# Kernel tuning notes

Measured on AMD Instinct MI355X. Metric: run time of the kernel, lower is better.

## Reference

```python
import jax, jax.numpy as jnp
import numpy as np

B, T, C = 128, 256, 384   # batch, seq (== BLOCK_SIZE), embed dim
H, D = 6, 64              # heads, head_dim
M = 128                   # memory prefix length
WIN = 64                  # local window


def setup_inputs() -> dict:
    key = jax.random.key(0)
    ks = jax.random.split(key, 6)
    s = 0.02
    return {
        "x": jax.random.normal(ks[0], (B, T, C), jnp.float32),
        "memory": jax.random.normal(ks[1], (M, C), jnp.float32),
        "W_qkv": (jax.random.normal(ks[2], (C, 3 * C), jnp.float32) * s),
        "b_qkv": jnp.zeros((3 * C,), jnp.float32),
        "W_proj": (jax.random.normal(ks[3], (C, C), jnp.float32) * s),
        "b_proj": jnp.zeros((C,), jnp.float32),
        "gate": jnp.ones((C,), jnp.float32),
    }


def reference(x, memory, W_qkv, b_qkv, W_proj, b_proj, gate):
    Bx, Tx, Cx = x.shape
    Mx = memory.shape[0]
    Tt = Tx + Mx

    qkv = x @ W_qkv + b_qkv                      # [B,T,3C]
    q, k, v = jnp.split(qkv, 3, axis=-1)
    mem = jnp.broadcast_to(memory[None], (Bx, Mx, Cx))
    k = jnp.concatenate([mem, k], axis=1)        # [B,Tt,C]
    v = jnp.concatenate([mem, v], axis=1)

    qh = q.reshape(Bx, Tx, H, D)
    kh = k.reshape(Bx, Tt, H, D)
    vh = v.reshape(Bx, Tt, H, D)

    att = jnp.einsum('bqhd,bkhd->bhqk', qh, kh) * (1.0 / jnp.sqrt(jnp.float32(D)))

    # self part (last T columns): causal AND local window; memory prefix unmasked
    i = jnp.arange(Tx)[:, None]
    j = jnp.arange(Tx)[None, :]
    self_mask = (j <= i) & (jnp.abs(i - j) <= WIN)            # [T,T]
    full_mask = jnp.concatenate(
        [jnp.ones((Tx, Mx), bool), self_mask], axis=1)        # [T,Tt]
    att = jnp.where(full_mask[None, None], att, -jnp.inf)
    att = jax.nn.softmax(att, axis=-1)

    y = jnp.einsum('bhqk,bkhd->bqhd', att, vh).reshape(Bx, Tx, Cx)
    return (y * gate) @ W_proj + b_proj
```

## Files before the change

### kernel.cpp

```cpp
#include <hip/hip_runtime.h>

#define B_   128
#define T_   256
#define C_   384
#define H_   6
#define D_   64
#define M_   128
#define WIN_ 64
#define C3_  1152
#define QKS_ 768

typedef unsigned int   uint;
typedef unsigned short ushort;
typedef __attribute__((ext_vector_type(8))) short bf16x8;
typedef __attribute__((ext_vector_type(4))) float f32x4;

#define AS1 __attribute__((address_space(1)))
#define AS3 __attribute__((address_space(3)))
#define MFMA16(a,b,c) __builtin_amdgcn_mfma_f32_16x16x32_bf16((a),(b),(c),0,0,0)

__device__ __forceinline__ ushort f2bf(float f) {
  union { float f; uint u; } c; c.f = f;
  uint x = c.u;
  return (ushort)((x + 0x7fffu + ((x >> 16) & 1u)) >> 16);
}
__device__ __forceinline__ void gload_lds16(const ushort* g, ushort* l) {
  __builtin_amdgcn_global_load_lds((const AS1 uint*)g, (AS3 uint*)l, 16, 0, 0);
}

#define NX4_  ((B_ * T_ * C_) / 4)
#define NM4_  ((M_ * C_) / 4)
#define NMT_  (H_ * 64 * 128)
#define NWQ_  (C_ * C3_)
#define NWP_  (C_ * C_)

__global__ __launch_bounds__(256)
void k_prep(const float* __restrict__ x, const float* __restrict__ memory,
            const float* __restrict__ Wq, const float* __restrict__ Wp,
            ushort* __restrict__ x_bf, ushort* __restrict__ mem_bf,
            ushort* __restrict__ memT, ushort* __restrict__ Wq_t,
            ushort* __restrict__ Wp_t)
{
  int id = blockIdx.x * 256 + threadIdx.x;
  if (id < NX4_) {
    float4 f = ((const float4*)x)[id];
    ushort4 u; u.x = f2bf(f.x); u.y = f2bf(f.y); u.z = f2bf(f.z); u.w = f2bf(f.w);
    *(ushort4*)&x_bf[id * 4] = u;
    return;
  }
  id -= NX4_;
  if (id < NM4_) {
    float4 f = ((const float4*)memory)[id];
    ushort4 u; u.x = f2bf(f.x); u.y = f2bf(f.y); u.z = f2bf(f.z); u.w = f2bf(f.w);
    *(ushort4*)&mem_bf[id * 4] = u;
    return;
  }
  id -= NM4_;
  if (id < NMT_) {
    int k = id & 127;
    int hd = id >> 7;
    int h = hd >> 6, d = hd & 63;
    memT[id] = f2bf(memory[(size_t)k * C_ + h * 64 + d]);
    return;
  }
  id -= NMT_;
  if (id < NWQ_) {
    int n = id / C_, k = id % C_;
    Wq_t[id] = f2bf(Wq[(size_t)k * C3_ + n]);
    return;
  }
  id -= NWQ_;
  if (id < NWP_) {
    int n = id / C_, k = id % C_;
    Wp_t[id] = f2bf(Wp[(size_t)k * C_ + n]);
  }
}

template<int MODE>
__global__ __launch_bounds__(256, 2)
void k_gemm(const ushort* __restrict__ A, const ushort* __restrict__ Bt,
            const float* __restrict__ bias, ushort* __restrict__ qkw,
            ushort* __restrict__ vTw, float* __restrict__ outf)
{
  __shared__ __align__(16) ushort smem[16384];
  constexpr int NT = MODE ? 3 : 9;
  const int wg = blockIdx.x;
  const int X = wg & 7, j = wg >> 3;
  const int bmT = X * 32 + j / NT;
  const int by = j - (j / NT) * NT;
  const int bm = bmT * 128, bn = by * 128;
  const int tid = threadIdx.x;
  const int lane = tid & 63, w = tid >> 6;
  const int wr = w >> 1, wc = w & 1;
  const int g = lane >> 4, l15 = lane & 15;

  f32x4 acc[4][4] = {};

  auto stage = [&](int buf, int k0) {
    #pragma unroll
    for (int i = 0; i < 2; ++i) {
      int s = i * 256 + tid;
      int row = s >> 2, cS = s & 3;
      int c = cS ^ ((row >> 1) & 3);
      gload_lds16(A  + (size_t)(bm + row) * C_ + k0 + c * 8, &smem[buf * 4096 + s * 8]);
      gload_lds16(Bt + (size_t)(bn + row) * C_ + k0 + c * 8, &smem[8192 + buf * 4096 + s * 8]);
    }
  };

  stage(0, 0);
  for (int t = 0; t < 12; ++t) {
    int cur = t & 1;
    if (t < 11) {
      stage(cur ^ 1, (t + 1) * 32);
      asm volatile("s_waitcnt vmcnt(4)" ::: "memory");
    } else {
      asm volatile("s_waitcnt vmcnt(0)" ::: "memory");
    }
    __builtin_amdgcn_s_barrier();

    bf16x8 af[4], bfr[4];
    #pragma unroll
    for (int m = 0; m < 4; ++m) {
      int row = wr * 64 + m * 16 + l15;
      int c = g ^ ((row >> 1) & 3);
      af[m] = *(const bf16x8*)&smem[cur * 4096 + row * 32 + c * 8];
    }
    #pragma unroll
    for (int n = 0; n < 4; ++n) {
      int row = wc * 64 + n * 16 + l15;
      int c = g ^ ((row >> 1) & 3);
      bfr[n] = *(const bf16x8*)&smem[8192 + cur * 4096 + row * 32 + c * 8];
    }
    #pragma unroll
    for (int m = 0; m < 4; ++m)
      #pragma unroll
      for (int n = 0; n < 4; ++n)
        acc[m][n] = MFMA16(af[m], bfr[n], acc[m][n]);

    __builtin_amdgcn_s_barrier();
  }

  if (MODE == 1) {
    #pragma unroll
    for (int m = 0; m < 4; ++m)
      #pragma unroll
      for (int n = 0; n < 4; ++n) {
        int col = bn + wc * 64 + n * 16 + l15;
        float bv = bias[col];
        #pragma unroll
        for (int r = 0; r < 4; ++r) {
          int row = bm + wr * 64 + m * 16 + g * 4 + r;
          outf[(size_t)row * C_ + col] = acc[m][n][r] + bv;
        }
      }
  } else if (by < 6) {
    #pragma unroll
    for (int m = 0; m < 4; ++m)
      #pragma unroll
      for (int n = 0; n < 4; ++n) {
        int col = bn + wc * 64 + n * 16 + l15;
        float bv = bias[col];
        #pragma unroll
        for (int r = 0; r < 4; ++r) {
          int row = bm + wr * 64 + m * 16 + g * 4 + r;
          qkw[(size_t)row * QKS_ + col] = f2bf(acc[m][n][r] + bv);
        }
      }
  } else {
    #pragma unroll
    for (int m = 0; m < 4; ++m)
      #pragma unroll
      for (int n = 0; n < 4; ++n) {
        int col = bn + wc * 64 + n * 16 + l15;
        int ch = col - 768, hh = ch >> 6, dd = ch & 63;
        float bv = bias[col];
        int row0 = bm + wr * 64 + m * 16 + g * 4;
        int bb = row0 >> 8, key0 = row0 & 255;
        uint lo = (uint)f2bf(acc[m][n][0] + bv) | ((uint)f2bf(acc[m][n][1] + bv) << 16);
        uint hi = (uint)f2bf(acc[m][n][2] + bv) | ((uint)f2bf(acc[m][n][3] + bv) << 16);
        uint2 uu; uu.x = lo; uu.y = hi;
        *(uint2*)(vTw + ((size_t)(bb * H_ + hh) * 64 + dd) * 256 + key0) = uu;
      }
  }
}

__global__ __launch_bounds__(256, 2)
void k_attn(const ushort* __restrict__ qkw, const ushort* __restrict__ vTw,
            const ushort* __restrict__ membf, const ushort* __restrict__ memT,
            const float* __restrict__ gate, ushort* __restrict__ y)
{
  __shared__ ushort Ks[2][384][32];
  __shared__ ushort Pb[4][64 * 32];

  const int b = blockIdx.x, h = blockIdx.y;
  const int tid = threadIdx.x, lane = tid & 63, w = tid >> 6;
  const int g = lane >> 4, l15 = lane & 15;
  const int q0 = w * 64;

  const ushort* qbase = qkw + (size_t)b * T_ * QKS_ + h * 64;
  const ushort* kcols = qbase + C_;
  const ushort* vbase = vTw + (size_t)(b * H_ + h) * 64 * 256;
  const ushort* mTb   = memT + (size_t)h * 64 * 128;

  #pragma unroll
  for (int i = 0; i < 12; ++i) {
    int s = i * 256 + tid;
    int kk = s / 1536, r4 = s - kk * 1536;
    int row = r4 >> 2, c8 = r4 & 3;
    int c = c8 ^ ((row >> 1) & 3);
    const ushort* src = (row < M_)
        ? membf + (size_t)row * C_ + h * 64 + kk * 32 + c * 8
        : kcols + (size_t)(row - M_) * QKS_ + kk * 32 + c * 8;
    gload_lds16(src, &Ks[0][0][0] + s * 8);
  }

  bf16x8 qf[4][2];
  #pragma unroll
  for (int m = 0; m < 4; ++m)
    #pragma unroll
    for (int kk = 0; kk < 2; ++kk)
      qf[m][kk] = *(const bf16x8*)(qbase + (size_t)(q0 + m * 16 + l15) * QKS_ + kk * 32 + g * 8);

  __syncthreads();

  f32x4 yacc[4][4] = {};
  float rsum[4][4] = {};
  ushort* P = &Pb[w][0];

  const int nch_self = (q0 == 0) ? 2 : 4;
  const int ss = M_ + ((q0 > WIN_) ? (q0 - WIN_) : 0);

  for (int ch = 0; ch < 4 + nch_self; ++ch) {
    const int r0 = (ch < 4) ? ch * 32 : ss + (ch - 4) * 32;
    const bool is_mem = (ch < 4);
    const ushort* vsrc = is_mem ? mTb : vbase;
    const int vld = is_mem ? 128 : 256;
    const int keyoff = is_mem ? r0 : (r0 - M_);

    f32x4 s_[4][2];
    #pragma unroll
    for (int m = 0; m < 4; ++m)
      #pragma unroll
      for (int n = 0; n < 2; ++n)
        s_[m][n] = (f32x4){0.f, 0.f, 0.f, 0.f};
    #pragma unroll
    for (int n = 0; n < 2; ++n) {
      int R = r0 + n * 16 + l15;
      int c = g ^ ((R >> 1) & 3);
      #pragma unroll
      for (int kk = 0; kk < 2; ++kk) {
        bf16x8 kf = *(const bf16x8*)&Ks[kk][R][c * 8];
        #pragma unroll
        for (int m = 0; m < 4; ++m)
          s_[m][n] = MFMA16(qf[m][kk], kf, s_[m][n]);
      }
    }

    #pragma unroll
    for (int m = 0; m < 4; ++m)
      #pragma unroll
      for (int n = 0; n < 2; ++n) {
        int key_row = r0 + n * 16 + l15;
        int jj = key_row - M_;
        int kc = n * 16 + l15;
        #pragma unroll
        for (int r = 0; r < 4; ++r) {
          int qi = q0 + m * 16 + g * 4 + r;
          bool ok = (key_row < M_) || ((jj <= qi) && (qi - jj <= WIN_));
          float p = ok ? __expf(s_[m][n][r] * 0.125f) : 0.f;
          rsum[m][r] += p;
          int ql = m * 16 + g * 4 + r;
          int sig = ((ql >> 1) ^ (ql >> 2)) & 3;
          P[ql * 32 + (kc ^ (sig << 3))] = f2bf(p);
        }
      }

    bf16x8 pa[4];
    #pragma unroll
    for (int m = 0; m < 4; ++m) {
      int row = m * 16 + l15;
      int sig = ((row >> 1) ^ (row >> 2)) & 3;
      pa[m] = *(const bf16x8*)&P[row * 32 + ((g ^ sig) << 3)];
    }
    #pragma unroll
    for (int n = 0; n < 4; ++n) {
      int dd = n * 16 + l15;
      bf16x8 vb = *(const bf16x8*)(vsrc + (size_t)dd * vld + keyoff + g * 8);
      #pragma unroll
      for (int m = 0; m < 4; ++m)
        yacc[m][n] = MFMA16(pa[m], vb, yacc[m][n]);
    }
  }

  float inv[4][4];
  #pragma unroll
  for (int m = 0; m < 4; ++m)
    #pragma unroll
    for (int r = 0; r < 4; ++r) {
      float v = rsum[m][r];
      v += __shfl_xor(v, 1); v += __shfl_xor(v, 2);
      v += __shfl_xor(v, 4); v += __shfl_xor(v, 8);
      inv[m][r] = 1.f / v;
    }

  #pragma unroll
  for (int m = 0; m < 4; ++m)
    #pragma unroll
    for (int n = 0; n < 4; ++n) {
      int dd = n * 16 + l15;
      float gv = gate[h * 64 + dd];
      #pragma unroll
      for (int r = 0; r < 4; ++r) {
        int qi = q0 + m * 16 + g * 4 + r;
        y[(size_t)(b * T_ + qi) * C_ + h * 64 + dd] = f2bf(yacc[m][n][r] * inv[m][r] * gv);
      }
    }
}

extern "C" void kernel_launch(void* const* d_in, const int* in_sizes, int n_in,
                              void* d_out, int out_size, void* d_ws, size_t ws_size,
                              hipStream_t stream) {
  const float* x      = (const float*)d_in[0];
  const float* memory = (const float*)d_in[1];
  const float* W_qkv  = (const float*)d_in[2];
  const float* b_qkv  = (const float*)d_in[3];
  const float* W_proj = (const float*)d_in[4];
  const float* b_proj = (const float*)d_in[5];
  const float* gate   = (const float*)d_in[6];
  float* out = (float*)d_out;

  ushort* p = (ushort*)d_ws;
  ushort* Wq_t  = p;  p += (size_t)C_ * C3_;
  ushort* Wp_t  = p;  p += (size_t)C_ * C_;
  ushort* membf = p;  p += (size_t)M_ * C_;
  ushort* memT  = p;  p += (size_t)NMT_;
  ushort* qkw   = p;  p += (size_t)B_ * T_ * QKS_;
  ushort* vTw   = p;  p += (size_t)B_ * T_ * C_;
  ushort* xybf  = p;  p += (size_t)B_ * T_ * C_;

  dim3 blk(256);

  int prep_items = NX4_ + NM4_ + NMT_ + NWQ_ + NWP_;
  k_prep<<<dim3((prep_items + 255) / 256), blk, 0, stream>>>(
      x, memory, W_qkv, W_proj, xybf, membf, memT, Wq_t, Wp_t);

  k_gemm<0><<<dim3(2304), blk, 0, stream>>>(xybf, Wq_t, b_qkv, qkw, vTw, nullptr);

  k_attn<<<dim3(B_, H_), blk, 0, stream>>>(qkw, vTw, membf, memT, gate, xybf);

  k_gemm<1><<<dim3(768), blk, 0, stream>>>(xybf, Wp_t, b_proj, nullptr, nullptr, out);
}
```

Measured before the change: 129.8 us.

## Read K directly from global in attention, drop LDS staging, raise occupancy

Removes the 48KB LDS staging buffer for K and the block-wide barrier, so each wave loads its K fragments straight from global memory, which is mostly cache-resident. Freeing LDS allows launch bounds to rise to 3 blocks per CU. The softmax exponent now uses exp2f with a prescaled constant, and bf16 packing uses the hardware v_cvt_pk_bf16_f32 instruction. The cost is redundant global/L2 reads of K across waves and stricter register limits that may cause spills.

```diff
diff --git a/kernel.cpp b/kernel.cpp
--- a/kernel.cpp
+++ b/kernel.cpp
@@ -23,6 +23,11 @@
   union { float f; uint u; } c; c.f = f;
   uint x = c.u;
   return (ushort)((x + 0x7fffu + ((x >> 16) & 1u)) >> 16);
+}
+__device__ __forceinline__ uint cvtpk(float lo, float hi) {
+  uint r;
+  asm("v_cvt_pk_bf16_f32 %0, %1, %2" : "=v"(r) : "v"(lo), "v"(hi));
+  return r;
 }
 __device__ __forceinline__ void gload_lds16(const ushort* g, ushort* l) {
   __builtin_amdgcn_global_load_lds((const AS1 uint*)g, (AS3 uint*)l, 16, 0, 0);
@@ -184,12 +189,11 @@
   }
 }
 
-__global__ __launch_bounds__(256, 2)
+__global__ __launch_bounds__(256, 3)
 void k_attn(const ushort* __restrict__ qkw, const ushort* __restrict__ vTw,
             const ushort* __restrict__ membf, const ushort* __restrict__ memT,
             const float* __restrict__ gate, ushort* __restrict__ y)
 {
-  __shared__ ushort Ks[2][384][32];
   __shared__ ushort Pb[4][64 * 32];
 
   const int b = blockIdx.x, h = blockIdx.y;
@@ -201,18 +205,7 @@
   const ushort* kcols = qbase + C_;
   const ushort* vbase = vTw + (size_t)(b * H_ + h) * 64 * 256;
   const ushort* mTb   = memT + (size_t)h * 64 * 128;
-
-  #pragma unroll
-  for (int i = 0; i < 12; ++i) {
-    int s = i * 256 + tid;
-    int kk = s / 1536, r4 = s - kk * 1536;
-    int row = r4 >> 2, c8 = r4 & 3;
-    int c = c8 ^ ((row >> 1) & 3);
-    const ushort* src = (row < M_)
-        ? membf + (size_t)row * C_ + h * 64 + kk * 32 + c * 8
-        : kcols + (size_t)(row - M_) * QKS_ + kk * 32 + c * 8;
-    gload_lds16(src, &Ks[0][0][0] + s * 8);
-  }
+  const ushort* mKb   = membf + h * 64;
 
   bf16x8 qf[4][2];
   #pragma unroll
@@ -221,8 +214,6 @@
     for (int kk = 0; kk < 2; ++kk)
       qf[m][kk] = *(const bf16x8*)(qbase + (size_t)(q0 + m * 16 + l15) * QKS_ + kk * 32 + g * 8);
 
-  __syncthreads();
-
   f32x4 yacc[4][4] = {};
   float rsum[4][4] = {};
   ushort* P = &Pb[w][0];
@@ -231,8 +222,11 @@
   const int ss = M_ + ((q0 > WIN_) ? (q0 - WIN_) : 0);
 
   for (int ch = 0; ch < 4 + nch_self; ++ch) {
-    const int r0 = (ch < 4) ? ch * 32 : ss + (ch - 4) * 32;
     const bool is_mem = (ch < 4);
+    const int r0 = is_mem ? ch * 32 : ss + (ch - 4) * 32;
+    const ushort* ksrc = is_mem ? (mKb + (size_t)r0 * C_)
+                                : (kcols + (size_t)(r0 - M_) * QKS_);
+    const int kstr = is_mem ? C_ : QKS_;
     const ushort* vsrc = is_mem ? mTb : vbase;
     const int vld = is_mem ? 128 : 256;
     const int keyoff = is_mem ? r0 : (r0 - M_);
@@ -245,11 +239,9 @@
         s_[m][n] = (f32x4){0.f, 0.f, 0.f, 0.f};
     #pragma unroll
     for (int n = 0; n < 2; ++n) {
-      int R = r0 + n * 16 + l15;
-      int c = g ^ ((R >> 1) & 3);
       #pragma unroll
       for (int kk = 0; kk < 2; ++kk) {
-        bf16x8 kf = *(const bf16x8*)&Ks[kk][R][c * 8];
+        bf16x8 kf = *(const bf16x8*)(ksrc + (size_t)(n * 16 + l15) * kstr + kk * 32 + g * 8);
         #pragma unroll
         for (int m = 0; m < 4; ++m)
           s_[m][n] = MFMA16(qf[m][kk], kf, s_[m][n]);
@@ -263,15 +255,24 @@
         int key_row = r0 + n * 16 + l15;
         int jj = key_row - M_;
         int kc = n * 16 + l15;
+        float p[4];
         #pragma unroll
         for (int r = 0; r < 4; ++r) {
           int qi = q0 + m * 16 + g * 4 + r;
           bool ok = (key_row < M_) || ((jj <= qi) && (qi - jj <= WIN_));
-          float p = ok ? __expf(s_[m][n][r] * 0.125f) : 0.f;
-          rsum[m][r] += p;
+          float e = ok ? exp2f(s_[m][n][r] * 0.18033688011112042f) : 0.f;
+          rsum[m][r] += e;
+          p[r] = e;
+        }
+        uint u01 = cvtpk(p[0], p[1]);
+        uint u23 = cvtpk(p[2], p[3]);
+        #pragma unroll
+        for (int r = 0; r < 4; ++r) {
           int ql = m * 16 + g * 4 + r;
           int sig = ((ql >> 1) ^ (ql >> 2)) & 3;
-          P[ql * 32 + (kc ^ (sig << 3))] = f2bf(p);
+          uint u = (r < 2) ? u01 : u23;
+          ushort val = (r & 1) ? (ushort)(u >> 16) : (ushort)(u & 0xffffu);
+          P[ql * 32 + (kc ^ (sig << 3))] = val;
         }
       }
 
```

After: 159.1 us. +22.6%, slower.
